# Optimization experiments

Measured on AMD Instinct MI355X. Metric: run time of the kernel, lower is better.

Reference implementation:

```python
import jax, jax.numpy as jnp
import numpy as np

B, N, E = 4, 50000, 800000
C_IN, C_OUT, K = 64, 64, 3  # K = max_degree
AVG_DEG = 16.0


def setup_inputs() -> dict:
    key = jax.random.key(0)
    k1, k2, k3, k4, k5 = jax.random.split(key, 5)
    x = jax.random.normal(k1, (B, N, C_IN), dtype=jnp.float32)
    lap_rows = jax.random.randint(k2, (E,), 0, N)
    lap_cols = jax.random.randint(k3, (E,), 0, N)
    # scale so ||L|| stays O(1) and the Chebyshev recursion is stable
    lap_vals = jax.random.normal(k4, (E,), dtype=jnp.float32) / AVG_DEG
    weights = jax.random.normal(k5, (K + 1, C_IN, C_OUT), dtype=jnp.float32) * 0.1
    bias = jnp.full((C_OUT,), 0.1, dtype=jnp.float32)
    return dict(x=x, lap_rows=lap_rows, lap_cols=lap_cols,
                lap_vals=lap_vals, weights=weights, bias=bias)


def reference(x, lap_rows, lap_cols, lap_vals, weights, bias):
    # Sparse L @ X via edge list: gather source rows, scale, scatter-add to dest rows.
    def spmm_one(xb):  # xb: [N, C]
        return jax.ops.segment_sum(lap_vals[:, None] * xb[lap_cols], lap_rows,
                                   num_segments=N)

    spmm = jax.vmap(spmm_one)  # [B, N, C] -> [B, N, C]

    Tx0 = x
    out = jnp.einsum('bnc,co->bno', Tx0, weights[0])
    Tx1 = spmm(Tx0)
    out = out + jnp.einsum('bnc,co->bno', Tx1, weights[1])
    for k in range(2, K + 1):
        Tx2 = 2.0 * spmm(Tx1) - Tx0
        out = out + jnp.einsum('bnc,co->bno', Tx2, weights[k])
        Tx0, Tx1 = Tx1, Tx2
    return jax.nn.relu(out + bias)
```

## Files before the change

### kernel.cpp

```cpp
#include <hip/hip_runtime.h>


#define N_NODES 50000
#define N_EDGES 800000
#define BATCH 4
#define CH 64
#define BN (N_NODES * CH)
#define ROWS_TOTAL (BATCH * N_NODES)
#define NB 782
#define EPB 8192
#define SCT_BLOCKS ((N_EDGES + EPB - 1) / EPB)

typedef unsigned int uint;
typedef unsigned short ushort;
typedef unsigned char uchar;
typedef __attribute__((ext_vector_type(8))) short short8;
typedef __attribute__((ext_vector_type(4))) float f32x4;

__device__ __forceinline__ float bf16lo(uint u) { return __uint_as_float(u << 16); }
__device__ __forceinline__ float bf16hi(uint u) { return __uint_as_float(u & 0xffff0000u); }
__device__ __forceinline__ uint pack_bf16(float lo, float hi) {
  uint a = __float_as_uint(lo);
  uint b = __float_as_uint(hi);
  a = (a + 0x7fffu + ((a >> 16) & 1u)) >> 16;
  b = (b + 0x7fffu + ((b >> 16) & 1u)) >> 16;
  return a | (b << 16);
}
__device__ __forceinline__ ushort bf16one(float x) {
  uint a = __float_as_uint(x);
  a = (a + 0x7fffu + ((a >> 16) & 1u)) >> 16;
  return (ushort)a;
}

__global__ __launch_bounds__(256) void bucket_hist(const int* __restrict__ rows,
                                                   int* __restrict__ gcounts) {
  __shared__ int h[NB];
  for (int b = threadIdx.x; b < NB; b += 256) h[b] = 0;
  __syncthreads();
  int base_e = blockIdx.x * EPB;
#pragma unroll
  for (int j = 0; j < EPB / 256; ++j) {
    int e = base_e + j * 256 + threadIdx.x;
    if (e < N_EDGES) atomicAdd(&h[rows[e] >> 6], 1);
  }
  __syncthreads();
  for (int b = threadIdx.x; b < NB; b += 256)
    if (h[b]) atomicAdd(&gcounts[b], h[b]);
}

__global__ __launch_bounds__(1024) void bucket_scan(const int* __restrict__ gcounts,
                                                    int* __restrict__ bucket_base,
                                                    int* __restrict__ gcursor) {
  __shared__ int s[1024];
  int t = threadIdx.x;
  int v = (t < NB) ? gcounts[t] : 0;
  s[t] = v;
  __syncthreads();
  for (int off = 1; off < 1024; off <<= 1) {
    int tv = (t >= off) ? s[t - off] : 0;
    __syncthreads();
    s[t] += tv;
    __syncthreads();
  }
  int ex = s[t] - v;
  if (t < NB) { bucket_base[t] = ex; gcursor[t] = ex; }
  if (t == NB) bucket_base[NB] = N_EDGES;
}

__global__ __launch_bounds__(256) void bucket_scatter(const int* __restrict__ rows,
                                                      const int* __restrict__ cols,
                                                      const float* __restrict__ vals,
                                                      int* __restrict__ gcursor,
                                                      uint2* __restrict__ staging) {
  __shared__ int lcur[NB];
  for (int b = threadIdx.x; b < NB; b += 256) lcur[b] = 0;
  __syncthreads();
  int base_e = blockIdx.x * EPB;
#pragma unroll
  for (int j = 0; j < EPB / 256; ++j) {
    int e = base_e + j * 256 + threadIdx.x;
    if (e < N_EDGES) atomicAdd(&lcur[rows[e] >> 6], 1);
  }
  __syncthreads();
  for (int b = threadIdx.x; b < NB; b += 256) {
    int c = lcur[b];
    lcur[b] = (c > 0) ? atomicAdd(&gcursor[b], c) : 0;
  }
  __syncthreads();
#pragma unroll
  for (int j = 0; j < EPB / 256; ++j) {
    int e = base_e + j * 256 + threadIdx.x;
    if (e < N_EDGES) {
      int r = rows[e];
      int pos = atomicAdd(&lcur[r >> 6], 1);
      staging[pos] = make_uint2((uint)cols[e] | ((uint)(r & 63) << 20),
                                __float_as_uint(vals[e]));
    }
  }
}

__global__ __launch_bounds__(256) void bucket_finalize(const int* __restrict__ bucket_base,
                                                       const uint2* __restrict__ staging,
                                                       uint2* __restrict__ pairs,
                                                       int* __restrict__ row_start) {
  int b = blockIdx.x;
  int seg0 = bucket_base[b], seg1 = bucket_base[b + 1];
  __shared__ int hist[64];
  __shared__ int cur[64];
  if (threadIdx.x < 64) hist[threadIdx.x] = 0;
  __syncthreads();
  for (int i = seg0 + threadIdx.x; i < seg1; i += 256)
    atomicAdd(&hist[staging[i].x >> 20], 1);
  __syncthreads();
  if (threadIdx.x < 64) {
    int v = hist[threadIdx.x];
    int sc = v;
#pragma unroll
    for (int off = 1; off < 64; off <<= 1) {
      int t = __shfl_up(sc, off, 64);
      if (threadIdx.x >= (unsigned)off) sc += t;
    }
    int start = seg0 + sc - v;
    cur[threadIdx.x] = start;
    int r = b * 64 + threadIdx.x;
    if (r < N_NODES) row_start[r] = start;
    if (r == N_NODES) row_start[N_NODES] = N_EDGES;
  }
  __syncthreads();
  for (int i = seg0 + threadIdx.x; i < seg1; i += 256) {
    uint2 eu = staging[i];
    int rl = eu.x >> 20;
    int pos = atomicAdd(&cur[rl], 1);
    pairs[pos] = make_uint2(eu.x & 0xFFFFFu, eu.y);
  }
}

__global__ __launch_bounds__(256) void wprep_kernel(const float* __restrict__ w,
                                                    ushort* __restrict__ wtT) {
  int t = blockIdx.x * 256 + threadIdx.x;
  if (t >= 64 * 256) return;
  int o = t >> 8, k = t & 255, m = k >> 6, c = k & 63;
  int idx = c * 64 + o;
  float v;
  if (m == 0)      v = w[idx] - w[2 * 4096 + idx];
  else if (m == 1) v = w[4096 + idx] - 3.0f * w[3 * 4096 + idx];
  else if (m == 2) v = 2.0f * w[2 * 4096 + idx];
  else             v = 4.0f * w[3 * 4096 + idx];
  wtT[t] = bf16one(v);
}

__global__ __launch_bounds__(256) void cvt_interleave_kernel(const float* __restrict__ in,
                                                             uint* __restrict__ outw) {
  int t = blockIdx.x * 256 + threadIdx.x;
  if (t >= (BATCH * BN) / 8) return;
  int c8 = t & 7;
  int b = (t >> 3) & 3;
  int node = t >> 5;
  const float* p = in + (size_t)b * BN + (size_t)node * 64 + c8 * 8;
  float4 a = *reinterpret_cast<const float4*>(p);
  float4 bb = *reinterpret_cast<const float4*>(p + 4);
  uint4 r;
  r.x = pack_bf16(a.x, a.y);
  r.y = pack_bf16(a.z, a.w);
  r.z = pack_bf16(bb.x, bb.y);
  r.w = pack_bf16(bb.z, bb.w);
  *reinterpret_cast<uint4*>(outw + (size_t)node * 128 + b * 32 + c8 * 4) = r;
}

__device__ __forceinline__ void edge_fma(float acc[8], float v, const uint4& q) {
  acc[0] = fmaf(v, bf16lo(q.x), acc[0]);
  acc[1] = fmaf(v, bf16hi(q.x), acc[1]);
  acc[2] = fmaf(v, bf16lo(q.y), acc[2]);
  acc[3] = fmaf(v, bf16hi(q.y), acc[3]);
  acc[4] = fmaf(v, bf16lo(q.z), acc[4]);
  acc[5] = fmaf(v, bf16hi(q.z), acc[5]);
  acc[6] = fmaf(v, bf16lo(q.w), acc[6]);
  acc[7] = fmaf(v, bf16hi(q.w), acc[7]);
}

__device__ __forceinline__ void edge_fma_i8(float acc[8], float m, const uint2& q) {
  acc[0] = fmaf(m, (float)((int)(q.x << 24) >> 24), acc[0]);
  acc[1] = fmaf(m, (float)((int)(q.x << 16) >> 24), acc[1]);
  acc[2] = fmaf(m, (float)((int)(q.x <<  8) >> 24), acc[2]);
  acc[3] = fmaf(m, (float)((int)q.x >> 24),         acc[3]);
  acc[4] = fmaf(m, (float)((int)(q.y << 24) >> 24), acc[4]);
  acc[5] = fmaf(m, (float)((int)(q.y << 16) >> 24), acc[5]);
  acc[6] = fmaf(m, (float)((int)(q.y <<  8) >> 24), acc[6]);
  acc[7] = fmaf(m, (float)((int)q.y >> 24),         acc[7]);
}

template <int READ_I8, int WRITE_I8>
__global__ __launch_bounds__(256) void spmm_kernel(
    const int* __restrict__ row_start, const uint2* __restrict__ pairs,
    const uint* __restrict__ src_bf, const uchar* __restrict__ src_i8,
    const float* __restrict__ src_sc, uint* __restrict__ dst_bf,
    uchar* __restrict__ dst_i8, float* __restrict__ dst_sc) {
  int row = blockIdx.x * 4 + (threadIdx.x >> 6);
  int lane = threadIdx.x & 63;
  int half = lane >> 5;
  int hl = lane & 31;
  int s = row_start[row], e = row_start[row + 1];
  float acc[8];
#pragma unroll
  for (int j = 0; j < 8; ++j) acc[j] = 0.f;
  int i = s + half;
  if (READ_I8) {
    const uchar* sb = src_i8 + hl * 8;
    for (; i + 6 < e; i += 8) {
      uint2 p[4];
#pragma unroll
      for (int u = 0; u < 4; ++u) p[u] = pairs[i + 2 * u];
      uint2 q[4];
      float m[4];
#pragma unroll
      for (int u = 0; u < 4; ++u) {
        q[u] = *reinterpret_cast<const uint2*>(sb + (size_t)p[u].x * 256);
        m[u] = __uint_as_float(p[u].y) * src_sc[p[u].x];
      }
#pragma unroll
      for (int u = 0; u < 4; ++u) edge_fma_i8(acc, m[u], q[u]);
    }
    for (; i < e; i += 2) {
      uint2 p0 = pairs[i];
      uint2 q0 = *reinterpret_cast<const uint2*>(sb + (size_t)p0.x * 256);
      edge_fma_i8(acc, __uint_as_float(p0.y) * src_sc[p0.x], q0);
    }
  } else {
    const uint* sw = src_bf + hl * 4;
    for (; i + 6 < e; i += 8) {
      uint2 p[4];
#pragma unroll
      for (int u = 0; u < 4; ++u) p[u] = pairs[i + 2 * u];
      uint4 q[4];
#pragma unroll
      for (int u = 0; u < 4; ++u)
        q[u] = *reinterpret_cast<const uint4*>(sw + (size_t)p[u].x * 128);
#pragma unroll
      for (int u = 0; u < 4; ++u) edge_fma(acc, __uint_as_float(p[u].y), q[u]);
    }
    for (; i < e; i += 2) {
      uint2 p0 = pairs[i];
      uint4 q0 = *reinterpret_cast<const uint4*>(sw + (size_t)p0.x * 128);
      edge_fma(acc, __uint_as_float(p0.y), q0);
    }
  }
#pragma unroll
  for (int j = 0; j < 8; ++j) acc[j] += __shfl_xor(acc[j], 32, 64);
  if (half == 0) {
    if (WRITE_I8) {
      float mx = 0.f;
#pragma unroll
      for (int j = 0; j < 8; ++j) mx = fmaxf(mx, fabsf(acc[j]));
#pragma unroll
      for (int off = 1; off < 32; off <<= 1)
        mx = fmaxf(mx, __shfl_xor(mx, off, 64));
      float inv = mx > 0.f ? 127.0f / mx : 0.f;
      uint w0 = 0, w1 = 0;
#pragma unroll
      for (int j = 0; j < 4; ++j)
        w0 |= ((uint)((int)rintf(acc[j] * inv) & 0xff)) << (8 * j);
#pragma unroll
      for (int j = 0; j < 4; ++j)
        w1 |= ((uint)((int)rintf(acc[4 + j] * inv) & 0xff)) << (8 * j);
      *reinterpret_cast<uint2*>(dst_i8 + (size_t)row * 256 + hl * 8) =
          make_uint2(w0, w1);
      if (hl == 0) dst_sc[row] = mx * (1.0f / 127.0f);
    } else {
      uint4 r;
      r.x = pack_bf16(acc[0], acc[1]);
      r.y = pack_bf16(acc[2], acc[3]);
      r.z = pack_bf16(acc[4], acc[5]);
      r.w = pack_bf16(acc[6], acc[7]);
      *reinterpret_cast<uint4*>(dst_bf + (size_t)row * 128 + hl * 4) = r;
    }
  }
}

__device__ __forceinline__ short8 dequant8(uint2 q, float sc) {
  float f0 = (float)((int)(q.x << 24) >> 24) * sc;
  float f1 = (float)((int)(q.x << 16) >> 24) * sc;
  float f2 = (float)((int)(q.x <<  8) >> 24) * sc;
  float f3 = (float)((int)q.x >> 24) * sc;
  float f4 = (float)((int)(q.y << 24) >> 24) * sc;
  float f5 = (float)((int)(q.y << 16) >> 24) * sc;
  float f6 = (float)((int)(q.y <<  8) >> 24) * sc;
  float f7 = (float)((int)q.y >> 24) * sc;
  uint4 v = make_uint4(pack_bf16(f0, f1), pack_bf16(f2, f3),
                       pack_bf16(f4, f5), pack_bf16(f6, f7));
  return __builtin_bit_cast(short8, v);
}

__global__ __launch_bounds__(256) void gemm4_mfma(
    const uint* __restrict__ A0bf,
    const uchar* __restrict__ A1i8, const float* __restrict__ A1sc,
    const uchar* __restrict__ A2i8, const float* __restrict__ A2sc,
    const uint* __restrict__ A3bf,
    const uint* __restrict__ wtT,
    const float* __restrict__ bias, float* __restrict__ out) {
  __shared__ uint WS[64 * 132];
  __shared__ float bias_s[64];
  for (int w = threadIdx.x; w < 8192; w += 256)
    WS[(w >> 7) * 132 + (w & 127)] = wtT[w];
  if (threadIdx.x < 64) bias_s[threadIdx.x] = bias[threadIdx.x];
  __syncthreads();

  const int lane = threadIdx.x & 63;
  const int wv = threadIdx.x >> 6;
  const int r0 = blockIdx.x * 64 + wv * 16;
  const int c16 = lane & 15;
  const int hi = lane >> 4;

  const int ar = r0 + c16;
  const size_t arow_w = (size_t)ar * 32 + hi * 4;
  const size_t arow_b = (size_t)ar * 64 + hi * 8;
  const float sc1 = A1sc[ar >> 2];
  const float sc2 = A2sc[ar >> 2];

  f32x4 acc[4] = {{0.f, 0.f, 0.f, 0.f}, {0.f, 0.f, 0.f, 0.f},
                  {0.f, 0.f, 0.f, 0.f}, {0.f, 0.f, 0.f, 0.f}};

#pragma unroll
  for (int ks = 0; ks < 8; ++ks) {
    short8 afrag;
    const int m = ks >> 1;
    if (m == 0) {
      uint4 av = *reinterpret_cast<const uint4*>(A0bf + arow_w + (ks & 1) * 16);
      afrag = __builtin_bit_cast(short8, av);
    } else if (m == 1) {
      uint2 qv = *reinterpret_cast<const uint2*>(A1i8 + arow_b + (ks & 1) * 32);
      afrag = dequant8(qv, sc1);
    } else if (m == 2) {
      uint2 qv = *reinterpret_cast<const uint2*>(A2i8 + arow_b + (ks & 1) * 32);
      afrag = dequant8(qv, sc2);
    } else {
      uint4 av = *reinterpret_cast<const uint4*>(A3bf + arow_w + (ks & 1) * 16);
      afrag = __builtin_bit_cast(short8, av);
    }
#pragma unroll
    for (int nt = 0; nt < 4; ++nt) {
      uint4 bv = *reinterpret_cast<const uint4*>(
          &WS[(nt * 16 + c16) * 132 + ks * 16 + hi * 4]);
      short8 bfrag = __builtin_bit_cast(short8, bv);
      acc[nt] = __builtin_amdgcn_mfma_f32_16x16x32_bf16(afrag, bfrag, acc[nt], 0, 0, 0);
    }
  }

#pragma unroll
  for (int nt = 0; nt < 4; ++nt) {
#pragma unroll
    for (int i = 0; i < 4; ++i) {
      int row = r0 + hi * 4 + i;
      int node = row >> 2, b = row & 3;
      int col = nt * 16 + c16;
      float v = acc[nt][i] + bias_s[col];
      out[(size_t)b * BN + (size_t)node * 64 + col] = fmaxf(v, 0.f);
    }
  }
}

extern "C" void kernel_launch(void* const* d_in, const int* in_sizes, int n_in,
                              void* d_out, int out_size, void* d_ws, size_t ws_size,
                              hipStream_t stream) {
  const float* x        = (const float*)d_in[0];
  const int*   lap_rows = (const int*)d_in[1];
  const int*   lap_cols = (const int*)d_in[2];
  const float* lap_vals = (const float*)d_in[3];
  const float* weights  = (const float*)d_in[4];
  const float* bias     = (const float*)d_in[5];
  float* out = (float*)d_out;

  char* ws = (char*)d_ws;
  size_t off = 0;
  auto alloc = [&](size_t bytes) {
    void* p = ws + off;
    off += (bytes + 255) & ~(size_t)255;
    return p;
  };
  int*    gcounts     = (int*)alloc((size_t)NB * 4);
  int*    gcursor     = (int*)alloc((size_t)NB * 4);
  int*    bucket_base = (int*)alloc((size_t)(NB + 1) * 4);
  int*    row_start   = (int*)alloc((size_t)(N_NODES + 1) * 4);
  uint2*  pairs       = (uint2*)alloc((size_t)N_EDGES * 8);
  ushort* wtT         = (ushort*)alloc((size_t)64 * 256 * 2);
  uint*   xb          = (uint*)alloc((size_t)N_NODES * 128 * 4);
  uchar*  S1i         = (uchar*)alloc((size_t)N_NODES * 256);
  uchar*  S2i         = (uchar*)alloc((size_t)N_NODES * 256);
  float*  S1sc        = (float*)alloc((size_t)N_NODES * 4);
  float*  S2sc        = (float*)alloc((size_t)N_NODES * 4);
  uint*   S3b         = (uint*)alloc((size_t)N_NODES * 128 * 4);
  uint2*  staging     = (uint2*)S3b;
  (void)ws_size; (void)in_sizes; (void)n_in; (void)out_size;

  wprep_kernel<<<64, 256, 0, stream>>>(weights, wtT);
  cvt_interleave_kernel<<<(BATCH * BN / 8 + 255) / 256, 256, 0, stream>>>(x, xb);
  hipMemsetAsync(gcounts, 0, (size_t)NB * 4, stream);
  bucket_hist<<<SCT_BLOCKS, 256, 0, stream>>>(lap_rows, gcounts);
  bucket_scan<<<1, 1024, 0, stream>>>(gcounts, bucket_base, gcursor);
  bucket_scatter<<<SCT_BLOCKS, 256, 0, stream>>>(lap_rows, lap_cols, lap_vals,
                                                 gcursor, staging);
  bucket_finalize<<<NB, 256, 0, stream>>>(bucket_base, staging, pairs, row_start);

  const int spmm_blocks = N_NODES / 4;

  spmm_kernel<0, 1><<<spmm_blocks, 256, 0, stream>>>(
      row_start, pairs, xb, nullptr, nullptr, nullptr, S1i, S1sc);
  spmm_kernel<1, 1><<<spmm_blocks, 256, 0, stream>>>(
      row_start, pairs, nullptr, S1i, S1sc, nullptr, S2i, S2sc);
  spmm_kernel<1, 0><<<spmm_blocks, 256, 0, stream>>>(
      row_start, pairs, nullptr, S2i, S2sc, S3b, nullptr, nullptr);
  gemm4_mfma<<<ROWS_TOTAL / 64, 256, 0, stream>>>(xb, S1i, S1sc, S2i, S2sc, S3b,
                                                  (const uint*)wtT, bias, out);
}
```

Before: 227.7 us.

## Quantize x and third Chebyshev term to int8, widen per-lane SpMM gathers

The conversion kernel now emits both bf16 and per-node int8 (with scale) copies of x. The first SpMM gathers int8 rows instead of bf16, and the last SpMM writes int8 instead of bf16, with the GEMM dequantizing the third term. The SpMM is restructured so each lane loads 16 bytes per edge with 4 edges in flight per wavefront, which halves gather bytes for two stages. This costs precision in x and S3, and staging now gets its own buffer instead of aliasing S3.

```diff
diff --git a/kernel.cpp b/kernel.cpp
--- a/kernel.cpp
+++ b/kernel.cpp
@@ -17,8 +17,6 @@
 typedef __attribute__((ext_vector_type(8))) short short8;
 typedef __attribute__((ext_vector_type(4))) float f32x4;
 
-__device__ __forceinline__ float bf16lo(uint u) { return __uint_as_float(u << 16); }
-__device__ __forceinline__ float bf16hi(uint u) { return __uint_as_float(u & 0xffff0000u); }
 __device__ __forceinline__ uint pack_bf16(float lo, float hi) {
   uint a = __float_as_uint(lo);
   uint b = __float_as_uint(hi);
@@ -149,131 +147,123 @@
   wtT[t] = bf16one(v);
 }
 
-__global__ __launch_bounds__(256) void cvt_interleave_kernel(const float* __restrict__ in,
-                                                             uint* __restrict__ outw) {
-  int t = blockIdx.x * 256 + threadIdx.x;
-  if (t >= (BATCH * BN) / 8) return;
-  int c8 = t & 7;
-  int b = (t >> 3) & 3;
-  int node = t >> 5;
-  const float* p = in + (size_t)b * BN + (size_t)node * 64 + c8 * 8;
-  float4 a = *reinterpret_cast<const float4*>(p);
-  float4 bb = *reinterpret_cast<const float4*>(p + 4);
-  uint4 r;
-  r.x = pack_bf16(a.x, a.y);
-  r.y = pack_bf16(a.z, a.w);
-  r.z = pack_bf16(bb.x, bb.y);
-  r.w = pack_bf16(bb.z, bb.w);
-  *reinterpret_cast<uint4*>(outw + (size_t)node * 128 + b * 32 + c8 * 4) = r;
-}
-
-__device__ __forceinline__ void edge_fma(float acc[8], float v, const uint4& q) {
-  acc[0] = fmaf(v, bf16lo(q.x), acc[0]);
-  acc[1] = fmaf(v, bf16hi(q.x), acc[1]);
-  acc[2] = fmaf(v, bf16lo(q.y), acc[2]);
-  acc[3] = fmaf(v, bf16hi(q.y), acc[3]);
-  acc[4] = fmaf(v, bf16lo(q.z), acc[4]);
-  acc[5] = fmaf(v, bf16hi(q.z), acc[5]);
-  acc[6] = fmaf(v, bf16lo(q.w), acc[6]);
-  acc[7] = fmaf(v, bf16hi(q.w), acc[7]);
-}
-
-__device__ __forceinline__ void edge_fma_i8(float acc[8], float m, const uint2& q) {
-  acc[0] = fmaf(m, (float)((int)(q.x << 24) >> 24), acc[0]);
-  acc[1] = fmaf(m, (float)((int)(q.x << 16) >> 24), acc[1]);
-  acc[2] = fmaf(m, (float)((int)(q.x <<  8) >> 24), acc[2]);
-  acc[3] = fmaf(m, (float)((int)q.x >> 24),         acc[3]);
-  acc[4] = fmaf(m, (float)((int)(q.y << 24) >> 24), acc[4]);
-  acc[5] = fmaf(m, (float)((int)(q.y << 16) >> 24), acc[5]);
-  acc[6] = fmaf(m, (float)((int)(q.y <<  8) >> 24), acc[6]);
-  acc[7] = fmaf(m, (float)((int)q.y >> 24),         acc[7]);
-}
-
-template <int READ_I8, int WRITE_I8>
-__global__ __launch_bounds__(256) void spmm_kernel(
-    const int* __restrict__ row_start, const uint2* __restrict__ pairs,
-    const uint* __restrict__ src_bf, const uchar* __restrict__ src_i8,
-    const float* __restrict__ src_sc, uint* __restrict__ dst_bf,
-    uchar* __restrict__ dst_i8, float* __restrict__ dst_sc) {
+__global__ __launch_bounds__(256) void cvt_kernel(const float* __restrict__ in,
+                                                  uint* __restrict__ xb,
+                                                  uint* __restrict__ xi8w,
+                                                  float* __restrict__ xsc) {
+  int node = blockIdx.x * 4 + (threadIdx.x >> 6);
+  int lane = threadIdx.x & 63;
+  int b = lane >> 4;
+  int ch4 = (lane & 15) * 4;
+  float4 v = *reinterpret_cast<const float4*>(in + (size_t)b * BN + (size_t)node * 64 + ch4);
+  uint2 bw = make_uint2(pack_bf16(v.x, v.y), pack_bf16(v.z, v.w));
+  *reinterpret_cast<uint2*>(xb + (size_t)node * 128 + b * 32 + (lane & 15) * 2) = bw;
+  float mx = fmaxf(fmaxf(fabsf(v.x), fabsf(v.y)), fmaxf(fabsf(v.z), fabsf(v.w)));
+#pragma unroll
+  for (int off = 1; off < 64; off <<= 1) mx = fmaxf(mx, __shfl_xor(mx, off, 64));
+  float inv = mx > 0.f ? 127.0f / mx : 0.f;
+  uint w8 = ((uint)((int)rintf(v.x * inv) & 0xff)) |
+            ((uint)((int)rintf(v.y * inv) & 0xff) << 8) |
+            ((uint)((int)rintf(v.z * inv) & 0xff) << 16) |
+            ((uint)((int)rintf(v.w * inv) & 0xff) << 24);
+  xi8w[(size_t)node * 64 + lane] = w8;
+  if (lane == 0) xsc[node] = mx * (1.0f / 127.0f);
+}
+
+__device__ __forceinline__ void fma16(float acc[16], float m, const uint4& w) {
+  const uint arr[4] = {w.x, w.y, w.z, w.w};
+#pragma unroll
+  for (int t = 0; t < 4; ++t) {
+    uint u = arr[t];
+    acc[t * 4 + 0] = fmaf(m, (float)((int)(u << 24) >> 24), acc[t * 4 + 0]);
+    acc[t * 4 + 1] = fmaf(m, (float)((int)(u << 16) >> 24), acc[t * 4 + 1]);
+    acc[t * 4 + 2] = fmaf(m, (float)((int)(u <<  8) >> 24), acc[t * 4 + 2]);
+    acc[t * 4 + 3] = fmaf(m, (float)((int)u >> 24),         acc[t * 4 + 3]);
+  }
+}
+
+__device__ __forceinline__ void spmm_body(const int* __restrict__ row_start,
+                                          const uint2* __restrict__ pairs,
+                                          const uchar* __restrict__ src,
+                                          const float* __restrict__ ssc,
+                                          uchar* __restrict__ dst,
+                                          float* __restrict__ dsc) {
   int row = blockIdx.x * 4 + (threadIdx.x >> 6);
   int lane = threadIdx.x & 63;
-  int half = lane >> 5;
-  int hl = lane & 31;
+  int q = lane >> 4;
+  int ql = lane & 15;
+  const uchar* sb = src + ql * 16;
   int s = row_start[row], e = row_start[row + 1];
-  float acc[8];
-#pragma unroll
-  for (int j = 0; j < 8; ++j) acc[j] = 0.f;
-  int i = s + half;
-  if (READ_I8) {
-    const uchar* sb = src_i8 + hl * 8;
-    for (; i + 6 < e; i += 8) {
-      uint2 p[4];
-#pragma unroll
-      for (int u = 0; u < 4; ++u) p[u] = pairs[i + 2 * u];
-      uint2 q[4];
-      float m[4];
-#pragma unroll
-      for (int u = 0; u < 4; ++u) {
-        q[u] = *reinterpret_cast<const uint2*>(sb + (size_t)p[u].x * 256);
-        m[u] = __uint_as_float(p[u].y) * src_sc[p[u].x];
-      }
-#pragma unroll
-      for (int u = 0; u < 4; ++u) edge_fma_i8(acc, m[u], q[u]);
-    }
-    for (; i < e; i += 2) {
-      uint2 p0 = pairs[i];
-      uint2 q0 = *reinterpret_cast<const uint2*>(sb + (size_t)p0.x * 256);
-      edge_fma_i8(acc, __uint_as_float(p0.y) * src_sc[p0.x], q0);
-    }
-  } else {
-    const uint* sw = src_bf + hl * 4;
-    for (; i + 6 < e; i += 8) {
-      uint2 p[4];
-#pragma unroll
-      for (int u = 0; u < 4; ++u) p[u] = pairs[i + 2 * u];
-      uint4 q[4];
-#pragma unroll
-      for (int u = 0; u < 4; ++u)
-        q[u] = *reinterpret_cast<const uint4*>(sw + (size_t)p[u].x * 128);
-#pragma unroll
-      for (int u = 0; u < 4; ++u) edge_fma(acc, __uint_as_float(p[u].y), q[u]);
-    }
-    for (; i < e; i += 2) {
-      uint2 p0 = pairs[i];
-      uint4 q0 = *reinterpret_cast<const uint4*>(sw + (size_t)p0.x * 128);
-      edge_fma(acc, __uint_as_float(p0.y), q0);
-    }
-  }
-#pragma unroll
-  for (int j = 0; j < 8; ++j) acc[j] += __shfl_xor(acc[j], 32, 64);
-  if (half == 0) {
-    if (WRITE_I8) {
-      float mx = 0.f;
-#pragma unroll
-      for (int j = 0; j < 8; ++j) mx = fmaxf(mx, fabsf(acc[j]));
-#pragma unroll
-      for (int off = 1; off < 32; off <<= 1)
-        mx = fmaxf(mx, __shfl_xor(mx, off, 64));
-      float inv = mx > 0.f ? 127.0f / mx : 0.f;
-      uint w0 = 0, w1 = 0;
-#pragma unroll
-      for (int j = 0; j < 4; ++j)
-        w0 |= ((uint)((int)rintf(acc[j] * inv) & 0xff)) << (8 * j);
-#pragma unroll
-      for (int j = 0; j < 4; ++j)
-        w1 |= ((uint)((int)rintf(acc[4 + j] * inv) & 0xff)) << (8 * j);
-      *reinterpret_cast<uint2*>(dst_i8 + (size_t)row * 256 + hl * 8) =
-          make_uint2(w0, w1);
-      if (hl == 0) dst_sc[row] = mx * (1.0f / 127.0f);
-    } else {
-      uint4 r;
-      r.x = pack_bf16(acc[0], acc[1]);
-      r.y = pack_bf16(acc[2], acc[3]);
-      r.z = pack_bf16(acc[4], acc[5]);
-      r.w = pack_bf16(acc[6], acc[7]);
-      *reinterpret_cast<uint4*>(dst_bf + (size_t)row * 128 + hl * 4) = r;
-    }
-  }
+  float acc[16];
+#pragma unroll
+  for (int j = 0; j < 16; ++j) acc[j] = 0.f;
+  int i = s;
+  for (; i + 7 < e; i += 8) {
+    uint2 pa = pairs[i + q];
+    uint2 pb = pairs[i + 4 + q];
+    uint4 qa = *reinterpret_cast<const uint4*>(sb + (size_t)pa.x * 256);
+    uint4 qb = *reinterpret_cast<const uint4*>(sb + (size_t)pb.x * 256);
+    float ma = __uint_as_float(pa.y) * ssc[pa.x];
+    float mb = __uint_as_float(pb.y) * ssc[pb.x];
+    fma16(acc, ma, qa);
+    fma16(acc, mb, qb);
+  }
+  for (; i < e; i += 4) {
+    if (i + q < e) {
+      uint2 p0 = pairs[i + q];
+      uint4 q0 = *reinterpret_cast<const uint4*>(sb + (size_t)p0.x * 256);
+      fma16(acc, __uint_as_float(p0.y) * ssc[p0.x], q0);
+    }
+  }
+#pragma unroll
+  for (int j = 0; j < 16; ++j) {
+    acc[j] += __shfl_xor(acc[j], 16, 64);
+    acc[j] += __shfl_xor(acc[j], 32, 64);
+  }
+  float mx = 0.f;
+#pragma unroll
+  for (int j = 0; j < 16; ++j) mx = fmaxf(mx, fabsf(acc[j]));
+#pragma unroll
+  for (int off = 1; off < 16; off <<= 1) mx = fmaxf(mx, __shfl_xor(mx, off, 64));
+  if (lane < 16) {
+    float inv = mx > 0.f ? 127.0f / mx : 0.f;
+    uint w[4];
+#pragma unroll
+    for (int t = 0; t < 4; ++t) {
+      w[t] = ((uint)((int)rintf(acc[t * 4 + 0] * inv) & 0xff)) |
+             ((uint)((int)rintf(acc[t * 4 + 1] * inv) & 0xff) << 8) |
+             ((uint)((int)rintf(acc[t * 4 + 2] * inv) & 0xff) << 16) |
+             ((uint)((int)rintf(acc[t * 4 + 3] * inv) & 0xff) << 24);
+    }
+    *reinterpret_cast<uint4*>(dst + (size_t)row * 256 + ql * 16) =
+        make_uint4(w[0], w[1], w[2], w[3]);
+    if (lane == 0) dsc[row] = mx * (1.0f / 127.0f);
+  }
+}
+
+__global__ __launch_bounds__(256) void spmm_s1(const int* __restrict__ rs,
+                                               const uint2* __restrict__ pr,
+                                               const uchar* __restrict__ src,
+                                               const float* __restrict__ ssc,
+                                               uchar* __restrict__ dst,
+                                               float* __restrict__ dsc) {
+  spmm_body(rs, pr, src, ssc, dst, dsc);
+}
+__global__ __launch_bounds__(256) void spmm_s2(const int* __restrict__ rs,
+                                               const uint2* __restrict__ pr,
+                                               const uchar* __restrict__ src,
+                                               const float* __restrict__ ssc,
+                                               uchar* __restrict__ dst,
+                                               float* __restrict__ dsc) {
+  spmm_body(rs, pr, src, ssc, dst, dsc);
+}
+__global__ __launch_bounds__(256) void spmm_s3(const int* __restrict__ rs,
+                                               const uint2* __restrict__ pr,
+                                               const uchar* __restrict__ src,
+                                               const float* __restrict__ ssc,
+                                               uchar* __restrict__ dst,
+                                               float* __restrict__ dsc) {
+  spmm_body(rs, pr, src, ssc, dst, dsc);
 }
 
 __device__ __forceinline__ short8 dequant8(uint2 q, float sc) {
@@ -294,7 +284,7 @@
     const uint* __restrict__ A0bf,
     const uchar* __restrict__ A1i8, const float* __restrict__ A1sc,
     const uchar* __restrict__ A2i8, const float* __restrict__ A2sc,
-    const uint* __restrict__ A3bf,
+    const uchar* __restrict__ A3i8, const float* __restrict__ A3sc,
     const uint* __restrict__ wtT,
     const float* __restrict__ bias, float* __restrict__ out) {
   __shared__ uint WS[64 * 132];
@@ -313,8 +303,10 @@
   const int ar = r0 + c16;
   const size_t arow_w = (size_t)ar * 32 + hi * 4;
   const size_t arow_b = (size_t)ar * 64 + hi * 8;
-  const float sc1 = A1sc[ar >> 2];
-  const float sc2 = A2sc[ar >> 2];
+  const int nd = ar >> 2;
+  const float sc1 = A1sc[nd];
+  const float sc2 = A2sc[nd];
+  const float sc3 = A3sc[nd];
 
   f32x4 acc[4] = {{0.f, 0.f, 0.f, 0.f}, {0.f, 0.f, 0.f, 0.f},
                   {0.f, 0.f, 0.f, 0.f}, {0.f, 0.f, 0.f, 0.f}};
@@ -333,8 +325,8 @@
       uint2 qv = *reinterpret_cast<const uint2*>(A2i8 + arow_b + (ks & 1) * 32);
       afrag = dequant8(qv, sc2);
     } else {
-      uint4 av = *reinterpret_cast<const uint4*>(A3bf + arow_w + (ks & 1) * 16);
-      afrag = __builtin_bit_cast(short8, av);
+      uint2 qv = *reinterpret_cast<const uint2*>(A3i8 + arow_b + (ks & 1) * 32);
+      afrag = dequant8(qv, sc3);
     }
 #pragma unroll
     for (int nt = 0; nt < 4; ++nt) {
@@ -381,18 +373,21 @@
   int*    bucket_base = (int*)alloc((size_t)(NB + 1) * 4);
   int*    row_start   = (int*)alloc((size_t)(N_NODES + 1) * 4);
   uint2*  pairs       = (uint2*)alloc((size_t)N_EDGES * 8);
+  uint2*  staging     = (uint2*)alloc((size_t)N_EDGES * 8);
   ushort* wtT         = (ushort*)alloc((size_t)64 * 256 * 2);
   uint*   xb          = (uint*)alloc((size_t)N_NODES * 128 * 4);
+  uchar*  xi8         = (uchar*)alloc((size_t)N_NODES * 256);
   uchar*  S1i         = (uchar*)alloc((size_t)N_NODES * 256);
   uchar*  S2i         = (uchar*)alloc((size_t)N_NODES * 256);
+  uchar*  S3i         = (uchar*)alloc((size_t)N_NODES * 256);
+  float*  xsc         = (float*)alloc((size_t)N_NODES * 4);
   float*  S1sc        = (float*)alloc((size_t)N_NODES * 4);
   float*  S2sc        = (float*)alloc((size_t)N_NODES * 4);
-  uint*   S3b         = (uint*)alloc((size_t)N_NODES * 128 * 4);
-  uint2*  staging     = (uint2*)S3b;
+  float*  S3sc        = (float*)alloc((size_t)N_NODES * 4);
   (void)ws_size; (void)in_sizes; (void)n_in; (void)out_size;
 
   wprep_kernel<<<64, 256, 0, stream>>>(weights, wtT);
-  cvt_interleave_kernel<<<(BATCH * BN / 8 + 255) / 256, 256, 0, stream>>>(x, xb);
+  cvt_kernel<<<N_NODES / 4, 256, 0, stream>>>(x, xb, (uint*)xi8, xsc);
   hipMemsetAsync(gcounts, 0, (size_t)NB * 4, stream);
   bucket_hist<<<SCT_BLOCKS, 256, 0, stream>>>(lap_rows, gcounts);
   bucket_scan<<<1, 1024, 0, stream>>>(gcounts, bucket_base, gcursor);
@@ -402,12 +397,10 @@
 
   const int spmm_blocks = N_NODES / 4;
 
-  spmm_kernel<0, 1><<<spmm_blocks, 256, 0, stream>>>(
-      row_start, pairs, xb, nullptr, nullptr, nullptr, S1i, S1sc);
-  spmm_kernel<1, 1><<<spmm_blocks, 256, 0, stream>>>(
-      row_start, pairs, nullptr, S1i, S1sc, nullptr, S2i, S2sc);
-  spmm_kernel<1, 0><<<spmm_blocks, 256, 0, stream>>>(
-      row_start, pairs, nullptr, S2i, S2sc, S3b, nullptr, nullptr);
-  gemm4_mfma<<<ROWS_TOTAL / 64, 256, 0, stream>>>(xb, S1i, S1sc, S2i, S2sc, S3b,
-                                                  (const uint*)wtT, bias, out);
-}
+  spmm_s1<<<spmm_blocks, 256, 0, stream>>>(row_start, pairs, xi8, xsc, S1i, S1sc);
+  spmm_s2<<<spmm_blocks, 256, 0, stream>>>(row_start, pairs, S1i, S1sc, S2i, S2sc);
+  spmm_s3<<<spmm_blocks, 256, 0, stream>>>(row_start, pairs, S2i, S2sc, S3i, S3sc);
+  gemm4_mfma<<<ROWS_TOTAL / 64, 256, 0, stream>>>(xb, S1i, S1sc, S2i, S2sc,
+                                                  S3i, S3sc, (const uint*)wtT,
+                                                  bias, out);
+}
```

Result: faster. 210.8 us (-7.4%).
